# Kernel tuning notes

Measured on AMD Instinct MI355X. Metric: run time of the kernel, lower is better.

Reference implementation:

```python
import jax, jax.numpy as jnp
import numpy as np

N_WIRES = 4
N_LAYERS = 3
N_PPL = 8  # n_params_per_layer
N_PATCH = 196  # 14*14 2x2 patches of a 28x28 image


def _expand(t, ndim):
    # right-pad singleton dims so t broadcasts against an array of rank `ndim`
    return t.reshape(t.shape + (1,) * (ndim - t.ndim))


def apply_ry(state, theta, wire):
    # state: (B, P, 2,2,2,2) complex; wire axis = 2 + wire (wire 0 = MSB, torchquantum convention)
    s = jnp.moveaxis(state, 2 + wire, -1)
    a0, a1 = s[..., 0], s[..., 1]
    th = jnp.asarray(theta, dtype=jnp.float32)
    c = _expand(jnp.cos(th / 2), a0.ndim)
    sn = _expand(jnp.sin(th / 2), a0.ndim)
    s = jnp.stack([c * a0 - sn * a1, sn * a0 + c * a1], axis=-1)
    return jnp.moveaxis(s, -1, 2 + wire)


def apply_rz(state, theta, wire):
    s = jnp.moveaxis(state, 2 + wire, -1)
    th = jnp.asarray(theta, dtype=jnp.float32)
    ph = jnp.exp(-0.5j * th.astype(jnp.complex64))
    ph = _expand(ph, s.ndim - 1)
    s = jnp.stack([ph * s[..., 0], jnp.conj(ph) * s[..., 1]], axis=-1)
    return jnp.moveaxis(s, -1, 2 + wire)


def apply_cx(state, control, target):
    s = jnp.moveaxis(state, (2 + control, 2 + target), (-2, -1))
    s = jnp.concatenate([s[..., 0:1, :], s[..., 1:2, ::-1]], axis=-2)
    return jnp.moveaxis(s, (-2, -1), (2 + control, 2 + target))


def extract_patches(x):
    # x: (B,1,28,28) -> (B,196,4) with pixel order [(r,c),(r,c+1),(r+1,c),(r+1,c+1)]
    B = x.shape[0]
    x = x.reshape(B, 28, 28).reshape(B, 14, 2, 14, 2)
    x = jnp.transpose(x, (0, 1, 3, 2, 4))  # (B,14,14,2,2)
    return x.reshape(B, N_PATCH, 4)


def simulate(data, vparams):
    # data: (B,P,4) encoder angles; vparams: (n_layers, n_params_per_layer)
    B, P, _ = data.shape
    state = jnp.zeros((B, P, 16), dtype=jnp.complex64).at[..., 0].set(1.0)
    state = state.reshape(B, P, 2, 2, 2, 2)
    # encoder: RY(data[w]) on wire w (GeneralEncoder resets to |0..0> first)
    for w in range(N_WIRES):
        state = apply_ry(state, data[..., w], w)
    # variational layers (parameter-shared across patches/batch)
    for l in range(N_LAYERS):
        p = vparams[l]
        for i in range(N_WIRES):
            state = apply_ry(state, p[i % N_PPL], i)
            state = apply_rz(state, p[(i + 1) % N_PPL], i)
        for i in range(N_WIRES):
            state = apply_cx(state, i, (i + 1) % N_WIRES)
    # <Z_w> for each wire
    probs = state.real ** 2 + state.imag ** 2  # (B,P,2,2,2,2)
    exps = []
    for w in range(N_WIRES):
        other = tuple(2 + a for a in range(N_WIRES) if a != w)
        pw = probs.sum(axis=other)  # (B,P,2)
        exps.append(pw[..., 0] - pw[..., 1])
    return jnp.stack(exps, axis=-1)  # (B,P,4)


def setup_inputs() -> dict:
    key = jax.random.key(0)
    k1, k2, k3 = jax.random.split(key, 3)
    B = 4096
    x = jax.random.uniform(k1, (B, 1, 28, 28), dtype=jnp.float32)
    vparams = jax.random.normal(k2, (N_LAYERS, N_PPL), dtype=jnp.float32)
    W = jax.random.normal(k3, (10, 4 * 14 * 14), dtype=jnp.float32) * 0.03
    b = jnp.zeros((10,), dtype=jnp.float32)
    return {"x": x, "vparams": vparams, "W": W, "b": b}


def reference(x, vparams, W, b):
    B = x.shape[0]
    data = extract_patches(x)                     # (B,196,4)
    feats = simulate(data, vparams).reshape(B, -1)  # (B,784), patch-major like torch.cat
    logits = feats @ W.T + b                      # (B,10)
    return jax.nn.log_softmax(logits, axis=-1)
```

## Files before the change

kernel.cpp:

```cpp
#include <hip/hip_runtime.h>
#include <hip/hip_bf16.h>


#define NPATCH 196

__global__ void qc_build_C(const float* __restrict__ vp,
                           float* __restrict__ Cout) {
  __shared__ float Ur[16][16];
  __shared__ float Ui[16][16];
  __shared__ float M[4][16][16];
  int t = threadIdx.x;

  if (t < 16) {
    float sr[16], si[16];
#pragma unroll
    for (int i = 0; i < 16; ++i) { sr[i] = 0.f; si[i] = 0.f; }
    sr[t] = 1.f;

    for (int l = 0; l < 3; ++l) {
#pragma unroll
      for (int w = 0; w < 4; ++w) {
        float thy = vp[l * 8 + (w % 8)];
        float thz = vp[l * 8 + ((w + 1) % 8)];
        float cy, sy, cz, sz;
        __sincosf(0.5f * thy, &sy, &cy);
        __sincosf(0.5f * thz, &sz, &cz);
        const int bit = 8 >> w;
#pragma unroll
        for (int i = 0; i < 16; ++i) {
          if (!(i & bit)) {
            int i1 = i | bit;
            float a0r = sr[i], a0i = si[i], a1r = sr[i1], a1i = si[i1];
            sr[i]  = cy * a0r - sy * a1r;  si[i]  = cy * a0i - sy * a1i;
            sr[i1] = sy * a0r + cy * a1r;  si[i1] = sy * a0i + cy * a1i;
          }
        }
#pragma unroll
        for (int i = 0; i < 16; ++i) {
          float r = sr[i], m = si[i];
          if (i & bit) { sr[i] = r * cz - m * sz; si[i] = m * cz + r * sz; }
          else         { sr[i] = r * cz + m * sz; si[i] = m * cz - r * sz; }
        }
      }
#pragma unroll
      for (int w = 0; w < 4; ++w) {
        const int cbit = 8 >> w;
        const int tbit = 8 >> ((w + 1) & 3);
#pragma unroll
        for (int i = 0; i < 16; ++i) {
          if ((i & cbit) && !(i & tbit)) {
            int i1 = i | tbit;
            float tr = sr[i], ti = si[i];
            sr[i] = sr[i1]; si[i] = si[i1];
            sr[i1] = tr;    si[i1] = ti;
          }
        }
      }
    }
#pragma unroll
    for (int i = 0; i < 16; ++i) { Ur[i][t] = sr[i]; Ui[i][t] = si[i]; }
  }
  __syncthreads();

  for (int e = t; e < 1024; e += 64) {
    int w = e >> 8, r = (e >> 4) & 15, c = e & 15;
    float acc = 0.f;
#pragma unroll
    for (int i = 0; i < 16; ++i) {
      float sgn = ((i >> (3 - w)) & 1) ? -1.f : 1.f;
      acc += sgn * (Ur[i][r] * Ur[i][c] + Ui[i][r] * Ui[i][c]);
    }
    M[w][r][c] = acc;
  }
  __syncthreads();

  const int pj1[10] = {0, 0, 0, 0, 1, 1, 1, 2, 2, 3};
  const int pj2[10] = {0, 1, 2, 3, 1, 2, 3, 2, 3, 3};
  for (int e = t; e < 400; e += 64) {
    int w = e / 100;
    int rem = e - w * 100;
    int a = rem / 10;
    int bq = rem - a * 10;
    int j1 = pj1[a], j2 = pj2[a], k1 = pj1[bq], k2 = pj2[bq];
    float v = M[w][4 * j1 + k1][4 * j2 + k2];
    if (k1 != k2) v += M[w][4 * j1 + k2][4 * j2 + k1];
    if (j1 != j2) {
      v += M[w][4 * j2 + k1][4 * j1 + k2];
      if (k1 != k2) v += M[w][4 * j2 + k2][4 * j1 + k1];
    }
    Cout[e] = v;
  }
}

__global__ __launch_bounds__(256) void qc_sim(const float* __restrict__ x,
                                              const float* __restrict__ C,
                                              float4* __restrict__ feats,
                                              int total) {
  int idx = blockIdx.x * 256 + threadIdx.x;
  if (idx >= total) return;
  int b = idx / 196;
  int p = idx - b * 196;
  int pr = p / 14;
  int pc = p - pr * 14;
  const float* xb = x + (size_t)b * 784;

  float2 top = *(const float2*)(xb + (2 * pr) * 28 + 2 * pc);
  float2 bot = *(const float2*)(xb + (2 * pr + 1) * 28 + 2 * pc);
  float s0, c0, s1, c1, s2, c2, s3, c3;
  __sincosf(0.5f * top.x, &s0, &c0);
  __sincosf(0.5f * top.y, &s1, &c1);
  __sincosf(0.5f * bot.x, &s2, &c2);
  __sincosf(0.5f * bot.y, &s3, &c3);

  float p0 = c0 * c1, p1 = c0 * s1, p2 = s0 * c1, p3 = s0 * s1;
  float q0 = c2 * c3, q1 = c2 * s3, q2 = s2 * c3, q3 = s2 * s3;

  float P[10] = {p0 * p0, p0 * p1, p0 * p2, p0 * p3, p1 * p1,
                 p1 * p2, p1 * p3, p2 * p2, p2 * p3, p3 * p3};
  float Q[10] = {q0 * q0, q0 * q1, q0 * q2, q0 * q3, q1 * q1,
                 q1 * q2, q1 * q3, q2 * q2, q2 * q3, q3 * q3};

  float e[4];
#pragma unroll
  for (int w = 0; w < 4; ++w) {
    float acc = 0.f;
#pragma unroll
    for (int a = 0; a < 10; ++a) {
      const float* row = C + (w * 10 + a) * 10;
      float tt = row[0] * Q[0] + row[1] * Q[1] + row[2] * Q[2] +
                 row[3] * Q[3] + row[4] * Q[4] + row[5] * Q[5] +
                 row[6] * Q[6] + row[7] * Q[7] + row[8] * Q[8] +
                 row[9] * Q[9];
      acc += P[a] * tt;
    }
    e[w] = acc;
  }
  feats[idx] = make_float4(e[0], e[1], e[2], e[3]);
}

__global__ __launch_bounds__(64) void qc_head(const float4* __restrict__ feats,
                                              const float4* __restrict__ W4,
                                              const float* __restrict__ bias,
                                              float* __restrict__ out) {
  int b = blockIdx.x;
  int lane = threadIdx.x;
  float lg[10];
#pragma unroll
  for (int c = 0; c < 10; ++c) lg[c] = 0.f;

  const float4* fb = feats + (size_t)b * NPATCH;
#pragma unroll
  for (int k = 0; k < 4; ++k) {
    int t = lane + 64 * k;
    if (t < NPATCH) {
      float4 f = fb[t];
#pragma unroll
      for (int c = 0; c < 10; ++c) {
        float4 w = W4[c * NPATCH + t];
        lg[c] += f.x * w.x + f.y * w.y + f.z * w.z + f.w * w.w;
      }
    }
  }
#pragma unroll
  for (int off = 32; off >= 1; off >>= 1)
#pragma unroll
    for (int c = 0; c < 10; ++c)
      lg[c] += __shfl_xor(lg[c], off, 64);

  if (lane == 0) {
    float L[10], m = -1e30f;
#pragma unroll
    for (int c = 0; c < 10; ++c) { L[c] = lg[c] + bias[c]; m = fmaxf(m, L[c]); }
    float ssum = 0.f;
#pragma unroll
    for (int c = 0; c < 10; ++c) ssum += __expf(L[c] - m);
    float ls = m + __logf(ssum);
#pragma unroll
    for (int c = 0; c < 10; ++c) out[b * 10 + c] = L[c] - ls;
  }
}

extern "C" void kernel_launch(void* const* d_in, const int* in_sizes, int n_in,
                              void* d_out, int out_size, void* d_ws, size_t ws_size,
                              hipStream_t stream) {
  const float* x    = (const float*)d_in[0];
  const float* vp   = (const float*)d_in[1];
  const float* W    = (const float*)d_in[2];
  const float* bias = (const float*)d_in[3];
  float* out = (float*)d_out;

  int B = in_sizes[0] / 784;

  float*  Cws   = (float*)d_ws;
  float4* feats = (float4*)((char*)d_ws + 2048);

  qc_build_C<<<1, 64, 0, stream>>>(vp, Cws);

  int total = B * NPATCH;
  qc_sim<<<(total + 255) / 256, 256, 0, stream>>>(x, Cws, feats, total);

  qc_head<<<B, 64, 0, stream>>>(feats, (const float4*)W, bias, out);
}
```

Measured before the change: 97.83 us.

## Fuse quantum simulation and linear head into one per-sample kernel

Merges the per-patch simulation kernel and the classifier head kernel into a single kernel with one 256-thread block per batch sample, one thread per patch. Per-patch features stay in registers and feed the W dot products directly, followed by wave shuffles and a shared-memory reduction across waves. This drops the global feats round trip and one kernel launch, at the cost of 60 idle threads per block and an added block-level sync.

```diff
diff --git a/kernel.cpp b/kernel.cpp
--- a/kernel.cpp
+++ b/kernel.cpp
@@ -92,85 +92,84 @@
   }
 }
 
-__global__ __launch_bounds__(256) void qc_sim(const float* __restrict__ x,
-                                              const float* __restrict__ C,
-                                              float4* __restrict__ feats,
-                                              int total) {
-  int idx = blockIdx.x * 256 + threadIdx.x;
-  if (idx >= total) return;
-  int b = idx / 196;
-  int p = idx - b * 196;
-  int pr = p / 14;
-  int pc = p - pr * 14;
-  const float* xb = x + (size_t)b * 784;
+__global__ __launch_bounds__(256) void qc_fused(const float* __restrict__ x,
+                                                const float* __restrict__ C,
+                                                const float4* __restrict__ W4,
+                                                const float* __restrict__ bias,
+                                                float* __restrict__ out) {
+  int b = blockIdx.x;
+  int p = threadIdx.x;
 
-  float2 top = *(const float2*)(xb + (2 * pr) * 28 + 2 * pc);
-  float2 bot = *(const float2*)(xb + (2 * pr + 1) * 28 + 2 * pc);
-  float s0, c0, s1, c1, s2, c2, s3, c3;
-  __sincosf(0.5f * top.x, &s0, &c0);
-  __sincosf(0.5f * top.y, &s1, &c1);
-  __sincosf(0.5f * bot.x, &s2, &c2);
-  __sincosf(0.5f * bot.y, &s3, &c3);
-
-  float p0 = c0 * c1, p1 = c0 * s1, p2 = s0 * c1, p3 = s0 * s1;
-  float q0 = c2 * c3, q1 = c2 * s3, q2 = s2 * c3, q3 = s2 * s3;
-
-  float P[10] = {p0 * p0, p0 * p1, p0 * p2, p0 * p3, p1 * p1,
-                 p1 * p2, p1 * p3, p2 * p2, p2 * p3, p3 * p3};
-  float Q[10] = {q0 * q0, q0 * q1, q0 * q2, q0 * q3, q1 * q1,
-                 q1 * q2, q1 * q3, q2 * q2, q2 * q3, q3 * q3};
-
-  float e[4];
-#pragma unroll
-  for (int w = 0; w < 4; ++w) {
-    float acc = 0.f;
-#pragma unroll
-    for (int a = 0; a < 10; ++a) {
-      const float* row = C + (w * 10 + a) * 10;
-      float tt = row[0] * Q[0] + row[1] * Q[1] + row[2] * Q[2] +
-                 row[3] * Q[3] + row[4] * Q[4] + row[5] * Q[5] +
-                 row[6] * Q[6] + row[7] * Q[7] + row[8] * Q[8] +
-                 row[9] * Q[9];
-      acc += P[a] * tt;
-    }
-    e[w] = acc;
-  }
-  feats[idx] = make_float4(e[0], e[1], e[2], e[3]);
-}
-
-__global__ __launch_bounds__(64) void qc_head(const float4* __restrict__ feats,
-                                              const float4* __restrict__ W4,
-                                              const float* __restrict__ bias,
-                                              float* __restrict__ out) {
-  int b = blockIdx.x;
-  int lane = threadIdx.x;
   float lg[10];
 #pragma unroll
   for (int c = 0; c < 10; ++c) lg[c] = 0.f;
 
-  const float4* fb = feats + (size_t)b * NPATCH;
+  if (p < NPATCH) {
+    int pr = p / 14;
+    int pc = p - pr * 14;
+    const float* xb = x + (size_t)b * 784;
+    float2 top = *(const float2*)(xb + (2 * pr) * 28 + 2 * pc);
+    float2 bot = *(const float2*)(xb + (2 * pr + 1) * 28 + 2 * pc);
+    float s0, c0, s1, c1, s2, c2, s3, c3;
+    __sincosf(0.5f * top.x, &s0, &c0);
+    __sincosf(0.5f * top.y, &s1, &c1);
+    __sincosf(0.5f * bot.x, &s2, &c2);
+    __sincosf(0.5f * bot.y, &s3, &c3);
+
+    float p0 = c0 * c1, p1 = c0 * s1, p2 = s0 * c1, p3 = s0 * s1;
+    float q0 = c2 * c3, q1 = c2 * s3, q2 = s2 * c3, q3 = s2 * s3;
+
+    float P[10] = {p0 * p0, p0 * p1, p0 * p2, p0 * p3, p1 * p1,
+                   p1 * p2, p1 * p3, p2 * p2, p2 * p3, p3 * p3};
+    float Q[10] = {q0 * q0, q0 * q1, q0 * q2, q0 * q3, q1 * q1,
+                   q1 * q2, q1 * q3, q2 * q2, q2 * q3, q3 * q3};
+
+    float e[4];
 #pragma unroll
-  for (int k = 0; k < 4; ++k) {
-    int t = lane + 64 * k;
-    if (t < NPATCH) {
-      float4 f = fb[t];
+    for (int w = 0; w < 4; ++w) {
+      float acc = 0.f;
 #pragma unroll
-      for (int c = 0; c < 10; ++c) {
-        float4 w = W4[c * NPATCH + t];
-        lg[c] += f.x * w.x + f.y * w.y + f.z * w.z + f.w * w.w;
+      for (int a = 0; a < 10; ++a) {
+        const float* row = C + (w * 10 + a) * 10;
+        float tt = row[0] * Q[0] + row[1] * Q[1] + row[2] * Q[2] +
+                   row[3] * Q[3] + row[4] * Q[4] + row[5] * Q[5] +
+                   row[6] * Q[6] + row[7] * Q[7] + row[8] * Q[8] +
+                   row[9] * Q[9];
+        acc += P[a] * tt;
       }
+      e[w] = acc;
+    }
+
+    float4 f = make_float4(e[0], e[1], e[2], e[3]);
+#pragma unroll
+    for (int c = 0; c < 10; ++c) {
+      float4 w = W4[c * NPATCH + p];
+      lg[c] = f.x * w.x + f.y * w.y + f.z * w.z + f.w * w.w;
     }
   }
+
 #pragma unroll
   for (int off = 32; off >= 1; off >>= 1)
 #pragma unroll
     for (int c = 0; c < 10; ++c)
       lg[c] += __shfl_xor(lg[c], off, 64);
 
+  __shared__ float red[4][10];
+  int wave = threadIdx.x >> 6;
+  int lane = threadIdx.x & 63;
   if (lane == 0) {
+#pragma unroll
+    for (int c = 0; c < 10; ++c) red[wave][c] = lg[c];
+  }
+  __syncthreads();
+
+  if (threadIdx.x == 0) {
     float L[10], m = -1e30f;
 #pragma unroll
-    for (int c = 0; c < 10; ++c) { L[c] = lg[c] + bias[c]; m = fmaxf(m, L[c]); }
+    for (int c = 0; c < 10; ++c) {
+      L[c] = red[0][c] + red[1][c] + red[2][c] + red[3][c] + bias[c];
+      m = fmaxf(m, L[c]);
+    }
     float ssum = 0.f;
 #pragma unroll
     for (int c = 0; c < 10; ++c) ssum += __expf(L[c] - m);
@@ -191,13 +190,9 @@
 
   int B = in_sizes[0] / 784;
 
-  float*  Cws   = (float*)d_ws;
-  float4* feats = (float4*)((char*)d_ws + 2048);
+  float* Cws = (float*)d_ws;
 
   qc_build_C<<<1, 64, 0, stream>>>(vp, Cws);
 
-  int total = B * NPATCH;
-  qc_sim<<<(total + 255) / 256, 256, 0, stream>>>(x, Cws, feats, total);
-
-  qc_head<<<B, 64, 0, stream>>>(feats, (const float4*)W, bias, out);
+  qc_fused<<<B, 256, 0, stream>>>(x, Cws, (const float4*)W, bias, out);
 }
```

Result: slower. 102.9 us (+5.2%).
